# Kernel optimization log

Hardware: AMD Instinct MI355X
Metric: run time of the kernel (lower is better)

## Reference

```python
import jax, jax.numpy as jnp
import numpy as np

N = 100000      # nodes
E = 1600000     # edges (before self-loops)
IN = 128        # in_dim
HID = 128       # hidden_dim
H = 4           # heads
D = HID // H    # head_dim = 32
L = 3           # n_layers
G = 128         # graphs in batch
NEG_SLOPE = 0.2 # PyG GATConv default leaky_relu slope
BN_EPS = 1e-5


def setup_inputs() -> dict:
    key = jax.random.key(0)
    ks = jax.random.split(key, 16)
    x = jax.random.normal(ks[0], (N, IN), dtype=jnp.float32)
    edge_index = jax.random.randint(ks[1], (2, E), 0, N, dtype=jnp.int64)
    batch = jnp.sort(jax.random.randint(ks[2], (N,), 0, G, dtype=jnp.int64))
    # stacked per-layer GATConv params (in_dim == hidden_dim so all layers stack)
    W = jax.random.normal(ks[3], (L, HID, HID), dtype=jnp.float32) * (1.0 / np.sqrt(HID))
    att_src = jax.random.normal(ks[4], (L, H, D), dtype=jnp.float32) * 0.1
    att_dst = jax.random.normal(ks[5], (L, H, D), dtype=jnp.float32) * 0.1
    bias = jax.random.normal(ks[6], (L, HID), dtype=jnp.float32) * 0.01
    # BatchNorm1d (eval mode: running stats)
    gamma = 1.0 + 0.1 * jax.random.normal(ks[7], (L, HID), dtype=jnp.float32)
    beta = 0.01 * jax.random.normal(ks[8], (L, HID), dtype=jnp.float32)
    bn_mean = jnp.zeros((L, HID), dtype=jnp.float32)
    bn_var = jnp.ones((L, HID), dtype=jnp.float32)
    # MLP head: Linear(HID, HID//2) -> ReLU -> Linear(HID//2, 1)
    Wh1 = jax.random.normal(ks[9], (HID, HID // 2), dtype=jnp.float32) * (1.0 / np.sqrt(HID))
    bh1 = jnp.zeros((HID // 2,), dtype=jnp.float32)
    Wh2 = jax.random.normal(ks[10], (HID // 2, 1), dtype=jnp.float32) * (1.0 / np.sqrt(HID // 2))
    bh2 = jnp.zeros((1,), dtype=jnp.float32)
    return {"x": x, "edge_index": edge_index, "batch": batch, "W": W,
            "att_src": att_src, "att_dst": att_dst, "bias": bias,
            "gamma": gamma, "beta": beta, "bn_mean": bn_mean, "bn_var": bn_var,
            "Wh1": Wh1, "bh1": bh1, "Wh2": Wh2, "bh2": bh2}


def _gat_conv(x, src, dst, W_l, asrc, adst, b):
    # x: [N, F_in]; src/dst: [E+N] (self-loops included); returns [N, H*D]
    h = (x @ W_l).reshape(N, H, D)                      # [N,H,D]
    a_s = jnp.einsum('nhd,hd->nh', h, asrc)             # [N,H]
    a_d = jnp.einsum('nhd,hd->nh', h, adst)
    e = jax.nn.leaky_relu(a_s[src] + a_d[dst], NEG_SLOPE)  # [Etot,H]
    # segment softmax over incoming edges per destination node
    e_max = jax.ops.segment_max(e, dst, num_segments=N)    # [N,H]
    p = jnp.exp(e - e_max[dst])
    denom = jax.ops.segment_sum(p, dst, num_segments=N)    # [N,H]
    alpha = p / (denom[dst] + 1e-16)                        # [Etot,H]
    msg = h[src] * alpha[:, :, None]                        # [Etot,H,D]
    out = jax.ops.segment_sum(msg, dst, num_segments=N)     # [N,H,D]
    return out.reshape(N, H * D) + b


def reference(x, edge_index, batch, W, att_src, att_dst, bias,
              gamma, beta, bn_mean, bn_var, Wh1, bh1, Wh2, bh2):
    # add self-loops once (PyG GATConv default add_self_loops=True)
    loop = jnp.arange(N, dtype=edge_index.dtype)
    src = jnp.concatenate([edge_index[0], loop])
    dst = jnp.concatenate([edge_index[1], loop])
    for l in range(L):
        x = _gat_conv(x, src, dst, W[l], att_src[l], att_dst[l], bias[l])
        x = jnp.maximum(x, 0.0)
        # BatchNorm1d, eval mode (dropout is identity in eval)
        x = (x - bn_mean[l]) * (gamma[l] / jnp.sqrt(bn_var[l] + BN_EPS)) + beta[l]
    # global mean pool over graphs
    sums = jax.ops.segment_sum(x, batch, num_segments=G)            # [G,HID]
    cnts = jax.ops.segment_sum(jnp.ones((N,), x.dtype), batch, num_segments=G)
    pooled = sums / jnp.maximum(cnts, 1.0)[:, None]
    hdn = jnp.maximum(pooled @ Wh1 + bh1, 0.0)
    return (hdn @ Wh2 + bh2).squeeze(-1)                            # [G]
```

## Files before the change

kernel.cpp:

```cpp
#include <hip/hip_runtime.h>
#include <hip/hip_fp16.h>


typedef __bf16 bf16x8 __attribute__((ext_vector_type(8)));
typedef float  f32x4  __attribute__((ext_vector_type(4)));
typedef unsigned int u32x4 __attribute__((ext_vector_type(4)));

#define WLSZ 36864
#define MAXBKT 800
#define BCAP   4096

__global__ __launch_bounds__(256)
void k_bucket(const int* __restrict__ ei, unsigned int* __restrict__ bkt,
              int* __restrict__ bcnt, float* __restrict__ gsum,
              int* __restrict__ gcnt, int Ne, int Nn, int nbkt, int Gg) {
    __shared__ int lcnt[MAXBKT];
    __shared__ int lbase[MAXBKT];
    int tid = threadIdx.x;
    int gid = blockIdx.x * 256 + tid;
    if (gid < Gg * 128) gsum[gid] = 0.f;
    if (gid < Gg) gcnt[gid] = 0;
    for (int i = tid; i < nbkt; i += 256) lcnt[i] = 0;
    __syncthreads();
    int chunk0 = blockIdx.x * 2048;
    int nnz = Ne + Nn;
    for (int i = 0; i < 8; ++i) {
        int e = chunk0 + i * 256 + tid;
        if (e < nnz) {
            int d = (e < Ne) ? ei[Ne + e] : (e - Ne);
            atomicAdd(&lcnt[d >> 7], 1);
        }
    }
    __syncthreads();
    for (int b = tid; b < nbkt; b += 256) {
        int c = lcnt[b];
        lbase[b] = (c > 0) ? atomicAdd(&bcnt[b], c) : 0;
        lcnt[b] = 0;
    }
    __syncthreads();
    for (int i = 0; i < 8; ++i) {
        int e = chunk0 + i * 256 + tid;
        if (e < nnz) {
            int s, d;
            if (e < Ne) { s = ei[e]; d = ei[Ne + e]; }
            else        { s = e - Ne; d = e - Ne; }
            int b = d >> 7;
            int r = atomicAdd(&lcnt[b], 1);
            bkt[(long)b * BCAP + lbase[b] + r] = ((unsigned)s << 7) | (unsigned)(d & 127);
        }
    }
}

__global__ __launch_bounds__(1024)
void k_bktscan(const int* __restrict__ bcnt, int* __restrict__ bktbase, int nbkt) {
    __shared__ int s0[1024], s1[1024];
    int t = threadIdx.x;
    int v = (t < nbkt) ? bcnt[t] : 0;
    s0[t] = v;
    __syncthreads();
    int* src = s0; int* dst = s1;
    for (int off = 1; off < 1024; off <<= 1) {
        int x = src[t];
        if (t >= off) x += src[t - off];
        dst[t] = x;
        __syncthreads();
        int* tw = src; src = dst; dst = tw;
    }
    if (t < nbkt) bktbase[t] = src[t] - v;
}

__global__ __launch_bounds__(256)
void k_bscatter2(const unsigned int* __restrict__ bkt, const int* __restrict__ bcnt,
                 const int* __restrict__ bktbase, int* __restrict__ rowptr,
                 int* __restrict__ colv, int Nn, int nnz) {
    __shared__ int h[128], sc0[128], sc1[128];
    int b = blockIdx.x;
    int tid = threadIdx.x;
    if (tid < 128) h[tid] = 0;
    __syncthreads();
    int cnt = bcnt[b];
    int base = bktbase[b];
    const unsigned int* bp = bkt + (long)b * BCAP;
    for (int i = tid; i < cnt; i += 256) atomicAdd(&h[bp[i] & 127], 1);
    __syncthreads();
    if (tid < 128) sc0[tid] = h[tid];
    __syncthreads();
    int* src = sc0; int* dst = sc1;
    for (int off = 1; off < 128; off <<= 1) {
        if (tid < 128) {
            int x = src[tid];
            if (tid >= off) x += src[tid - off];
            dst[tid] = x;
        }
        __syncthreads();
        int* tw = src; src = dst; dst = tw;
    }
    int node = b * 128 + tid;
    if (tid < 128) {
        int excl = src[tid] - h[tid];
        int st = base + excl;
        h[tid] = st;
        if (node < Nn) rowptr[node] = st;
    }
    if (b == 0 && tid == 0) rowptr[Nn] = nnz;
    __syncthreads();
    for (int i = tid; i < cnt; i += 256) {
        unsigned int e = bp[i];
        int pos = atomicAdd(&h[e & 127], 1);
        colv[pos] = (int)(e >> 7);
    }
}

__device__ __forceinline__ int foff(int l, int d, int n, int k) {
    int ct = n >> 4, li = n & 15;
    int ks = k >> 5, bq = (k >> 3) & 3, j = k & 7;
    return l * WLSZ + (((ks * 18) + d * 9 + ct) * 64 + (bq << 4) + li) * 8 + j;
}

__global__ void k_prep(const float* __restrict__ gamma, const float* __restrict__ beta,
                       const float* __restrict__ mean, const float* __restrict__ var,
                       float* __restrict__ bn_mul, float* __restrict__ bn_add,
                       const float* __restrict__ W, const float* __restrict__ asrc,
                       const float* __restrict__ adst, __bf16* __restrict__ WF) {
    int gid = blockIdx.x * 256 + threadIdx.x;
    if (gid < 384) {
        float sc = gamma[gid] / sqrtf(var[gid] + 1e-5f);
        bn_mul[gid] = sc;
        bn_add[gid] = beta[gid] - mean[gid] * sc;
    }
    if (gid < 3 * 128 * 128) {
        int l = gid >> 14;
        int k = (gid >> 7) & 127;
        int n = gid & 127;
        float f = W[gid];
        __bf16 h = (__bf16)f;
        WF[foff(l, 0, n, k)] = h;
        WF[foff(l, 1, n, k)] = (__bf16)(f - (float)h);
    }
    if (gid < 3 * 128 * 8) {
        int l = gid >> 10;
        int r = gid & 1023;
        int k = r >> 3;
        int j = r & 7;
        int hh = j & 3;
        const float* av = (j < 4 ? asrc : adst) + l * 128 + hh * 32;
        const float* wp = W + l * 16384 + k * 128 + hh * 32;
        float sum = 0.f;
#pragma unroll
        for (int d = 0; d < 32; ++d) sum = fmaf(wp[d], av[d], sum);
        __bf16 h = (__bf16)sum;
        WF[foff(l, 0, 128 + j, k)] = h;
        WF[foff(l, 1, 128 + j, k)] = (__bf16)(sum - (float)h);
    }
    if (gid < 3 * 128 * 8) {
        int l = gid >> 10;
        int r = gid & 1023;
        int k = r >> 3;
        int j = r & 7;
        WF[foff(l, 0, 136 + j, k)] = (__bf16)0.f;
        WF[foff(l, 1, 136 + j, k)] = (__bf16)0.f;
    }
}

__global__ __launch_bounds__(256, 4)
void k_gemm_mfma(const float* __restrict__ X, const __bf16* __restrict__ WF,
                 __half* __restrict__ Hout,
                 float* __restrict__ as_, float* __restrict__ ad_, int Nn) {
    int t = threadIdx.x;
    int w = t >> 6;
    int lane = t & 63;
    int li = lane & 15;
    int b  = lane >> 4;
    long row = (long)blockIdx.x * 64 + w * 16 + li;
    long rA = (row > Nn - 1) ? (Nn - 1) : row;

    f32x4 acc[9];
#pragma unroll
    for (int ct = 0; ct < 9; ++ct) acc[ct] = (f32x4){0.f, 0.f, 0.f, 0.f};

#pragma unroll
    for (int ks = 0; ks < 4; ++ks) {
        int k0 = ks * 32 + 8 * b;
        const float* xp = X + rA * 128 + k0;
        float4 f0 = *(const float4*)xp;
        float4 f1 = *(const float4*)(xp + 4);
        float af[8] = {f0.x, f0.y, f0.z, f0.w, f1.x, f1.y, f1.z, f1.w};
        bf16x8 ahi, alo;
#pragma unroll
        for (int j = 0; j < 8; ++j) {
            __bf16 h = (__bf16)af[j];
            ahi[j] = h;
            alo[j] = (__bf16)(af[j] - (float)h);
        }
        const __bf16* wk = WF + (ks * 18) * 512 + lane * 8;
#pragma unroll
        for (int ct = 0; ct < 9; ++ct) {
            bf16x8 bhi = *(const bf16x8*)(wk + ct * 512);
            bf16x8 blo = *(const bf16x8*)(wk + (9 + ct) * 512);
            acc[ct] = __builtin_amdgcn_mfma_f32_16x16x32_bf16(bhi, ahi, acc[ct], 0, 0, 0);
            acc[ct] = __builtin_amdgcn_mfma_f32_16x16x32_bf16(bhi, alo, acc[ct], 0, 0, 0);
            acc[ct] = __builtin_amdgcn_mfma_f32_16x16x32_bf16(blo, ahi, acc[ct], 0, 0, 0);
        }
    }

    if (row < Nn) {
        __half* op = Hout + row * 128 + 4 * b;
#pragma unroll
        for (int ct = 0; ct < 8; ++ct) {
            union { __half2 h2[2]; uint2 u; } pk;
            pk.h2[0] = __floats2half2_rn(acc[ct][0], acc[ct][1]);
            pk.h2[1] = __floats2half2_rn(acc[ct][2], acc[ct][3]);
            *(uint2*)(op + ct * 16) = pk.u;
        }
        if (b == 0)
            *(float4*)(as_ + 4 * row) = make_float4(acc[8][0], acc[8][1],
                                                    acc[8][2], acc[8][3]);
        else if (b == 1)
            *(float4*)(ad_ + 4 * row) = make_float4(acc[8][0], acc[8][1],
                                                    acc[8][2], acc[8][3]);
    }
}

#define LEAKY(x) ((x) > 0.f ? (x) : 0.2f * (x))

__global__ __launch_bounds__(256)
void k_aggregate(const __half* __restrict__ Hb, const float* __restrict__ as_,
                 const float* __restrict__ ad_, const int* __restrict__ rowptr,
                 const int* __restrict__ col, const float* __restrict__ bias,
                 const float* __restrict__ bn_mul, const float* __restrict__ bn_add,
                 float* __restrict__ Xout, int Nn) {
    __shared__ int2 s_pk[4][64][4];
    int w = threadIdx.x >> 6;
    int n = (blockIdx.x << 2) + w;
    if (n >= Nn) return;
    int lane = threadIdx.x & 63;
    int start = rowptr[n], end = rowptr[n + 1];
    int deg = end - start;

    if (deg <= 64) {
        int hh = lane & 3;
        int slot = lane >> 2;
        float adn = ad_[4 * n + hh];
        float esc[4]; int scl[4];
#pragma unroll
        for (int c = 0; c < 4; ++c) {
            int eidx = (c << 4) + slot;
            float e = -1e30f; int s = 0;
            if (eidx < deg) {
                s = col[start + eidx];
                e = LEAKY(as_[4 * s + hh] + adn);
            }
            esc[c] = e; scl[c] = s;
        }
        float m = fmaxf(fmaxf(esc[0], esc[1]), fmaxf(esc[2], esc[3]));
#pragma unroll
        for (int msk = 4; msk < 64; msk <<= 1) m = fmaxf(m, __shfl_xor(m, msk, 64));
        float p[4];
        float den = 0.f;
#pragma unroll
        for (int c = 0; c < 4; ++c) { p[c] = __expf(esc[c] - m); den += p[c]; }
#pragma unroll
        for (int msk = 4; msk < 64; msk <<= 1) den += __shfl_xor(den, msk, 64);
        float inv = 1.f / (den + 1e-16f);
#pragma unroll
        for (int c = 0; c < 4; ++c) {
            int2 pk;
            pk.x = scl[c] << 8;
            pk.y = __float_as_int(p[c] * inv);
            s_pk[w][(c << 4) + slot][hh] = pk;
        }

        int quarter = lane >> 4;
        int li = lane & 15;
        int hB = li >> 2;
        int cByte = li << 4;
        const char* hb8 = (const char*)Hb;
        float acc[8];
#pragma unroll
        for (int i = 0; i < 8; ++i) acc[i] = 0.f;

        int nit = (deg + 7) >> 3;
        int2 pk0 = s_pk[w][quarter][hB];
        int2 pk1 = s_pk[w][quarter + 4][hB];
        float a0 = __int_as_float(pk0.y);
        float a1 = __int_as_float(pk1.y);
        u32x4 r0 = *(const u32x4*)(hb8 + pk0.x + cByte);
        u32x4 r1 = *(const u32x4*)(hb8 + pk1.x + cByte);
        for (int it = 1; it < nit; ++it) {
            int e0 = (it << 3) + quarter;
            int2 q0 = s_pk[w][e0][hB];
            int2 q1 = s_pk[w][e0 + 4][hB];
            u32x4 t0 = *(const u32x4*)(hb8 + q0.x + cByte);
            u32x4 t1 = *(const u32x4*)(hb8 + q1.x + cByte);
            const __half* h0 = (const __half*)&r0;
            const __half* h1 = (const __half*)&r1;
#pragma unroll
            for (int q = 0; q < 8; ++q) {
                acc[q] = fmaf(__half2float(h0[q]), a0, acc[q]);
                acc[q] = fmaf(__half2float(h1[q]), a1, acc[q]);
            }
            r0 = t0; r1 = t1;
            a0 = __int_as_float(q0.y);
            a1 = __int_as_float(q1.y);
        }
        {
            const __half* h0 = (const __half*)&r0;
            const __half* h1 = (const __half*)&r1;
#pragma unroll
            for (int q = 0; q < 8; ++q) {
                acc[q] = fmaf(__half2float(h0[q]), a0, acc[q]);
                acc[q] = fmaf(__half2float(h1[q]), a1, acc[q]);
            }
        }
#pragma unroll
        for (int i = 0; i < 8; ++i) {
            float v = acc[i];
            v += __shfl_xor(v, 16, 64);
            v += __shfl_xor(v, 32, 64);
            acc[i] = v;
        }
        if (lane < 16) {
            int c0 = li << 3;
            float4 bz0 = *(const float4*)(bias + c0);
            float4 bz1 = *(const float4*)(bias + c0 + 4);
            float4 m0 = *(const float4*)(bn_mul + c0);
            float4 m1 = *(const float4*)(bn_mul + c0 + 4);
            float4 a0v = *(const float4*)(bn_add + c0);
            float4 a1v = *(const float4*)(bn_add + c0 + 4);
            float4 o0, o1;
            o0.x = fmaf(fmaxf(acc[0] + bz0.x, 0.f), m0.x, a0v.x);
            o0.y = fmaf(fmaxf(acc[1] + bz0.y, 0.f), m0.y, a0v.y);
            o0.z = fmaf(fmaxf(acc[2] + bz0.z, 0.f), m0.z, a0v.z);
            o0.w = fmaf(fmaxf(acc[3] + bz0.w, 0.f), m0.w, a0v.w);
            o1.x = fmaf(fmaxf(acc[4] + bz1.x, 0.f), m1.x, a1v.x);
            o1.y = fmaf(fmaxf(acc[5] + bz1.y, 0.f), m1.y, a1v.y);
            o1.z = fmaf(fmaxf(acc[6] + bz1.z, 0.f), m1.z, a1v.z);
            o1.w = fmaf(fmaxf(acc[7] + bz1.w, 0.f), m1.w, a1v.w);
            *(float4*)(Xout + (long)n * 128 + c0)     = o0;
            *(float4*)(Xout + (long)n * 128 + c0 + 4) = o1;
        }
        return;
    }

    int hh = lane & 3;
    float adn = ad_[n * 4 + hh];
    float m = -1e30f;
    for (int base = start; base < end; base += 16) {
        int idx = base + (lane >> 2);
        float sc = -1e30f;
        if (idx < end) {
            int s = col[idx];
            float e = as_[s * 4 + hh] + adn;
            sc = LEAKY(e);
        }
        m = fmaxf(m, sc);
    }
    for (int msk = 4; msk < 64; msk <<= 1) m = fmaxf(m, __shfl_xor(m, msk, 64));
    float den = 0.f;
    for (int base = start; base < end; base += 16) {
        int idx = base + (lane >> 2);
        if (idx < end) {
            int s = col[idx];
            float e = as_[s * 4 + hh] + adn;
            e = LEAKY(e);
            den += __expf(e - m);
        }
    }
    for (int msk = 4; msk < 64; msk <<= 1) den += __shfl_xor(den, msk, 64);
    int hB = lane >> 4;
    float mB   = __shfl(m, hB, 64);
    float invB = 1.f / (__shfl(den, hB, 64) + 1e-16f);
    float adB  = ad_[n * 4 + hB];
    int c0 = lane << 1;
    float acc0 = 0.f, acc1 = 0.f;
    for (int i = start; i < end; ++i) {
        int s = col[i];
        float e = as_[s * 4 + hB] + adB;
        e = LEAKY(e);
        float alpha = __expf(e - mB) * invB;
        float2 hv = __half22float2(*(const __half2*)(Hb + (long)s * 128 + c0));
        acc0 = fmaf(hv.x, alpha, acc0);
        acc1 = fmaf(hv.y, alpha, acc1);
    }
    float v0 = acc0 + bias[c0], v1 = acc1 + bias[c0 + 1];
    v0 = fmaxf(v0, 0.f); v1 = fmaxf(v1, 0.f);
    v0 = fmaf(v0, bn_mul[c0], bn_add[c0]);
    v1 = fmaf(v1, bn_mul[c0 + 1], bn_add[c0 + 1]);
    *(float2*)(Xout + (long)n * 128 + c0) = make_float2(v0, v1);
}

__global__ __launch_bounds__(128)
void k_pool(const float* __restrict__ X, const int* __restrict__ batch,
            float* __restrict__ gsum, int* __restrict__ gcnt, int Nn) {
    int c = threadIdx.x;
    int n0 = blockIdx.x * 64;
    if (n0 >= Nn) return;
    int nend = (n0 + 64 < Nn) ? n0 + 64 : Nn;
    float local = 0.f;
    int gcur = batch[n0];
    int cnt = 0;
    for (int n = n0; n < nend; ++n) {
        int g = batch[n];
        if (g != gcur) {
            atomicAdd(&gsum[gcur * 128 + c], local);
            if (c == 0) atomicAdd(&gcnt[gcur], cnt);
            local = 0.f; cnt = 0; gcur = g;
        }
        local += X[(long)n * 128 + c];
        cnt += 1;
    }
    atomicAdd(&gsum[gcur * 128 + c], local);
    if (c == 0) atomicAdd(&gcnt[gcur], cnt);
}

__global__ __launch_bounds__(64)
void k_head(const float* __restrict__ gsum, const int* __restrict__ gcnt,
            const float* __restrict__ Wh1, const float* __restrict__ bh1,
            const float* __restrict__ Wh2, const float* __restrict__ bh2,
            float* __restrict__ outp) {
    __shared__ float pooled[128];
    int g = blockIdx.x;
    int j = threadIdx.x;
    int cnt = gcnt[g];
    float inv = 1.f / (float)(cnt > 1 ? cnt : 1);
    pooled[j]      = gsum[g * 128 + j] * inv;
    pooled[j + 64] = gsum[g * 128 + 64 + j] * inv;
    __syncthreads();
    float acc = bh1[j];
    for (int k = 0; k < 128; ++k) acc = fmaf(pooled[k], Wh1[k * 64 + j], acc);
    acc = fmaxf(acc, 0.f);
    float prod = acc * Wh2[j];
    for (int msk = 1; msk < 64; msk <<= 1) prod += __shfl_xor(prod, msk, 64);
    if (j == 0) outp[g] = prod + bh2[0];
}

extern "C" void kernel_launch(void* const* d_in, const int* in_sizes, int n_in,
                              void* d_out, int out_size, void* d_ws, size_t ws_size,
                              hipStream_t stream) {
    const float* x       = (const float*)d_in[0];
    const int*   ei      = (const int*)d_in[1];
    const int*   batch   = (const int*)d_in[2];
    const float* W       = (const float*)d_in[3];
    const float* att_src = (const float*)d_in[4];
    const float* att_dst = (const float*)d_in[5];
    const float* bias    = (const float*)d_in[6];
    const float* gamma   = (const float*)d_in[7];
    const float* beta    = (const float*)d_in[8];
    const float* bn_mean = (const float*)d_in[9];
    const float* bn_var  = (const float*)d_in[10];
    const float* Wh1     = (const float*)d_in[11];
    const float* bh1     = (const float*)d_in[12];
    const float* Wh2     = (const float*)d_in[13];
    const float* bh2     = (const float*)d_in[14];
    float* out = (float*)d_out;

    const int Nn = in_sizes[0] / 128;
    const int Ne = in_sizes[1] / 2;
    const int Gg = out_size;
    const int nnz = Ne + Nn;
    const int nbkt = (Nn + 127) / 128;

    char* ws = (char*)d_ws;
    size_t off = 0;
    auto alloc = [&](size_t bytes) -> char* {
        char* p = ws + off;
        off = (off + bytes + 255) & ~(size_t)255;
        return p;
    };
    float*        bufA    = (float*)alloc((size_t)Nn * 128 * 4);
    __half*       bufH    = (__half*)alloc((size_t)Nn * 128 * 2);
    float*        as_     = (float*)alloc((size_t)Nn * 4 * 4);
    float*        ad_     = (float*)alloc((size_t)Nn * 4 * 4);
    int*          rowptr  = (int*)alloc((size_t)(Nn + 1) * 4);
    int*          col     = (int*)alloc((size_t)nnz * 4);
    float*        bn_mul  = (float*)alloc(384 * 4);
    float*        bn_add  = (float*)alloc(384 * 4);
    float*        gsum    = (float*)alloc((size_t)Gg * 128 * 4);
    int*          gcnt    = (int*)alloc((size_t)Gg * 4);
    __bf16*       WtF     = (__bf16*)alloc((size_t)3 * WLSZ * 2);
    unsigned int* bkt     = (unsigned int*)alloc((size_t)nbkt * BCAP * 4);
    int*          bcnt    = (int*)alloc((size_t)nbkt * 4);
    int*          bktbase = (int*)alloc((size_t)nbkt * 4);

    hipMemsetAsync(bcnt, 0, (size_t)nbkt * 4, stream);
    k_prep<<<192, 256, 0, stream>>>(gamma, beta, bn_mean, bn_var, bn_mul, bn_add,
                                    W, att_src, att_dst, WtF);
    k_bucket<<<(nnz + 2047) / 2048, 256, 0, stream>>>(ei, bkt, bcnt, gsum, gcnt,
                                                      Ne, Nn, nbkt, Gg);
    k_bktscan<<<1, 1024, 0, stream>>>(bcnt, bktbase, nbkt);
    k_bscatter2<<<nbkt, 256, 0, stream>>>(bkt, bcnt, bktbase, rowptr, col, Nn, nnz);

    const float* cur = x;
    for (int l = 0; l < 3; ++l) {
        k_gemm_mfma<<<(Nn + 63) / 64, 256, 0, stream>>>(cur, WtF + l * WLSZ,
                                                        bufH, as_, ad_, Nn);
        k_aggregate<<<(Nn + 3) / 4, 256, 0, stream>>>(bufH, as_, ad_, rowptr, col,
                                                      bias + l * 128, bn_mul + l * 128,
                                                      bn_add + l * 128, bufA, Nn);
        cur = bufA;
    }

    k_pool<<<(Nn + 63) / 64, 128, 0, stream>>>(bufA, batch, gsum, gcnt, Nn);
    k_head<<<Gg, 64, 0, stream>>>(gsum, gcnt, Wh1, bh1, Wh2, bh2, out);
}
```

Baseline: 524.2 us.

## Fuse global mean pooling into last-layer aggregation and compute graph counts by binary search

The final aggregation kernel becomes a template with a pooling variant. For the last layer it no longer writes the 100000x128 activation matrix. Each block instead stages its four node outputs in shared memory and atomically adds them into per-graph sums, merging them into one add when all four nodes share a graph. Graph node counts come from a small binary-search kernel over the sorted batch array, which removes the separate pool kernel and its full re-read of the activations. The cost is an extra __syncthreads plus up to 128 global atomics per block, which will contend heavily on only 128 graphs.

```diff
diff --git a/kernel.cpp b/kernel.cpp
--- a/kernel.cpp
+++ b/kernel.cpp
@@ -111,6 +111,17 @@
     }
 }
 
+__global__ __launch_bounds__(128)
+void k_gcnt(const int* __restrict__ batch, int* __restrict__ gcnt, int Nn, int Gg) {
+    int g = threadIdx.x;
+    if (g >= Gg) return;
+    int lo = 0, hi = Nn;
+    while (lo < hi) { int mid = (lo + hi) >> 1; if (batch[mid] < g) lo = mid + 1; else hi = mid; }
+    int lo2 = lo, hi2 = Nn;
+    while (lo2 < hi2) { int mid = (lo2 + hi2) >> 1; if (batch[mid] < g + 1) lo2 = mid + 1; else hi2 = mid; }
+    gcnt[g] = lo2 - lo;
+}
+
 __device__ __forceinline__ int foff(int l, int d, int n, int k) {
     int ct = n >> 4, li = n & 15;
     int ks = k >> 5, bq = (k >> 3) & 3, j = k & 7;
@@ -223,194 +234,212 @@
 
 #define LEAKY(x) ((x) > 0.f ? (x) : 0.2f * (x))
 
+template <bool POOL>
 __global__ __launch_bounds__(256)
 void k_aggregate(const __half* __restrict__ Hb, const float* __restrict__ as_,
                  const float* __restrict__ ad_, const int* __restrict__ rowptr,
                  const int* __restrict__ col, const float* __restrict__ bias,
                  const float* __restrict__ bn_mul, const float* __restrict__ bn_add,
-                 float* __restrict__ Xout, int Nn) {
+                 float* __restrict__ Xout, const int* __restrict__ batch,
+                 float* __restrict__ gsum, int Nn) {
     __shared__ int2 s_pk[4][64][4];
+    __shared__ float s_out[POOL ? 4 : 1][POOL ? 128 : 1];
+    __shared__ int s_g[POOL ? 4 : 1];
     int w = threadIdx.x >> 6;
     int n = (blockIdx.x << 2) + w;
-    if (n >= Nn) return;
     int lane = threadIdx.x & 63;
-    int start = rowptr[n], end = rowptr[n + 1];
-    int deg = end - start;
-
-    if (deg <= 64) {
-        int hh = lane & 3;
-        int slot = lane >> 2;
-        float adn = ad_[4 * n + hh];
-        float esc[4]; int scl[4];
-#pragma unroll
-        for (int c = 0; c < 4; ++c) {
-            int eidx = (c << 4) + slot;
-            float e = -1e30f; int s = 0;
-            if (eidx < deg) {
-                s = col[start + eidx];
-                e = LEAKY(as_[4 * s + hh] + adn);
-            }
-            esc[c] = e; scl[c] = s;
-        }
-        float m = fmaxf(fmaxf(esc[0], esc[1]), fmaxf(esc[2], esc[3]));
-#pragma unroll
-        for (int msk = 4; msk < 64; msk <<= 1) m = fmaxf(m, __shfl_xor(m, msk, 64));
-        float p[4];
-        float den = 0.f;
-#pragma unroll
-        for (int c = 0; c < 4; ++c) { p[c] = __expf(esc[c] - m); den += p[c]; }
-#pragma unroll
-        for (int msk = 4; msk < 64; msk <<= 1) den += __shfl_xor(den, msk, 64);
-        float inv = 1.f / (den + 1e-16f);
-#pragma unroll
-        for (int c = 0; c < 4; ++c) {
-            int2 pk;
-            pk.x = scl[c] << 8;
-            pk.y = __float_as_int(p[c] * inv);
-            s_pk[w][(c << 4) + slot][hh] = pk;
-        }
-
-        int quarter = lane >> 4;
-        int li = lane & 15;
-        int hB = li >> 2;
-        int cByte = li << 4;
-        const char* hb8 = (const char*)Hb;
-        float acc[8];
-#pragma unroll
-        for (int i = 0; i < 8; ++i) acc[i] = 0.f;
-
-        int nit = (deg + 7) >> 3;
-        int2 pk0 = s_pk[w][quarter][hB];
-        int2 pk1 = s_pk[w][quarter + 4][hB];
-        float a0 = __int_as_float(pk0.y);
-        float a1 = __int_as_float(pk1.y);
-        u32x4 r0 = *(const u32x4*)(hb8 + pk0.x + cByte);
-        u32x4 r1 = *(const u32x4*)(hb8 + pk1.x + cByte);
-        for (int it = 1; it < nit; ++it) {
-            int e0 = (it << 3) + quarter;
-            int2 q0 = s_pk[w][e0][hB];
-            int2 q1 = s_pk[w][e0 + 4][hB];
-            u32x4 t0 = *(const u32x4*)(hb8 + q0.x + cByte);
-            u32x4 t1 = *(const u32x4*)(hb8 + q1.x + cByte);
-            const __half* h0 = (const __half*)&r0;
-            const __half* h1 = (const __half*)&r1;
-#pragma unroll
-            for (int q = 0; q < 8; ++q) {
-                acc[q] = fmaf(__half2float(h0[q]), a0, acc[q]);
-                acc[q] = fmaf(__half2float(h1[q]), a1, acc[q]);
-            }
-            r0 = t0; r1 = t1;
-            a0 = __int_as_float(q0.y);
-            a1 = __int_as_float(q1.y);
-        }
-        {
-            const __half* h0 = (const __half*)&r0;
-            const __half* h1 = (const __half*)&r1;
-#pragma unroll
-            for (int q = 0; q < 8; ++q) {
-                acc[q] = fmaf(__half2float(h0[q]), a0, acc[q]);
-                acc[q] = fmaf(__half2float(h1[q]), a1, acc[q]);
-            }
-        }
-#pragma unroll
-        for (int i = 0; i < 8; ++i) {
-            float v = acc[i];
-            v += __shfl_xor(v, 16, 64);
-            v += __shfl_xor(v, 32, 64);
-            acc[i] = v;
-        }
+    bool active = (n < Nn);
+    if (!POOL && !active) return;
+    if (POOL && lane == 0) s_g[w] = active ? batch[n] : -1;
+
+    if (active) {
+        int start = rowptr[n], end = rowptr[n + 1];
+        int deg = end - start;
+
+        if (deg <= 64) {
+            int hh = lane & 3;
+            int slot = lane >> 2;
+            float adn = ad_[4 * n + hh];
+            float esc[4]; int scl[4];
+#pragma unroll
+            for (int c = 0; c < 4; ++c) {
+                int eidx = (c << 4) + slot;
+                float e = -1e30f; int s = 0;
+                if (eidx < deg) {
+                    s = col[start + eidx];
+                    e = LEAKY(as_[4 * s + hh] + adn);
+                }
+                esc[c] = e; scl[c] = s;
+            }
+            float m = fmaxf(fmaxf(esc[0], esc[1]), fmaxf(esc[2], esc[3]));
+#pragma unroll
+            for (int msk = 4; msk < 64; msk <<= 1) m = fmaxf(m, __shfl_xor(m, msk, 64));
+            float p[4];
+            float den = 0.f;
+#pragma unroll
+            for (int c = 0; c < 4; ++c) { p[c] = __expf(esc[c] - m); den += p[c]; }
+#pragma unroll
+            for (int msk = 4; msk < 64; msk <<= 1) den += __shfl_xor(den, msk, 64);
+            float inv = 1.f / (den + 1e-16f);
+#pragma unroll
+            for (int c = 0; c < 4; ++c) {
+                int2 pk;
+                pk.x = scl[c] << 8;
+                pk.y = __float_as_int(p[c] * inv);
+                s_pk[w][(c << 4) + slot][hh] = pk;
+            }
+
+            int quarter = lane >> 4;
+            int li = lane & 15;
+            int hB = li >> 2;
+            int cByte = li << 4;
+            const char* hb8 = (const char*)Hb;
+            float acc[8];
+#pragma unroll
+            for (int i = 0; i < 8; ++i) acc[i] = 0.f;
+
+            int nit = (deg + 7) >> 3;
+            int2 pk0 = s_pk[w][quarter][hB];
+            int2 pk1 = s_pk[w][quarter + 4][hB];
+            float a0 = __int_as_float(pk0.y);
+            float a1 = __int_as_float(pk1.y);
+            u32x4 r0 = *(const u32x4*)(hb8 + pk0.x + cByte);
+            u32x4 r1 = *(const u32x4*)(hb8 + pk1.x + cByte);
+            for (int it = 1; it < nit; ++it) {
+                int e0 = (it << 3) + quarter;
+                int2 q0 = s_pk[w][e0][hB];
+                int2 q1 = s_pk[w][e0 + 4][hB];
+                u32x4 t0 = *(const u32x4*)(hb8 + q0.x + cByte);
+                u32x4 t1 = *(const u32x4*)(hb8 + q1.x + cByte);
+                const __half* h0 = (const __half*)&r0;
+                const __half* h1 = (const __half*)&r1;
+#pragma unroll
+                for (int q = 0; q < 8; ++q) {
+                    acc[q] = fmaf(__half2float(h0[q]), a0, acc[q]);
+                    acc[q] = fmaf(__half2float(h1[q]), a1, acc[q]);
+                }
+                r0 = t0; r1 = t1;
+                a0 = __int_as_float(q0.y);
+                a1 = __int_as_float(q1.y);
+            }
+            {
+                const __half* h0 = (const __half*)&r0;
+                const __half* h1 = (const __half*)&r1;
+#pragma unroll
+                for (int q = 0; q < 8; ++q) {
+                    acc[q] = fmaf(__half2float(h0[q]), a0, acc[q]);
+                    acc[q] = fmaf(__half2float(h1[q]), a1, acc[q]);
+                }
+            }
+#pragma unroll
+            for (int i = 0; i < 8; ++i) {
+                float v = acc[i];
+                v += __shfl_xor(v, 16, 64);
+                v += __shfl_xor(v, 32, 64);
+                acc[i] = v;
+            }
+            if (lane < 16) {
+                int c0 = li << 3;
+                float4 bz0 = *(const float4*)(bias + c0);
+                float4 bz1 = *(const float4*)(bias + c0 + 4);
+                float4 m0 = *(const float4*)(bn_mul + c0);
+                float4 m1 = *(const float4*)(bn_mul + c0 + 4);
+                float4 a0v = *(const float4*)(bn_add + c0);
+                float4 a1v = *(const float4*)(bn_add + c0 + 4);
+                float4 o0, o1;
+                o0.x = fmaf(fmaxf(acc[0] + bz0.x, 0.f), m0.x, a0v.x);
+                o0.y = fmaf(fmaxf(acc[1] + bz0.y, 0.f), m0.y, a0v.y);
+                o0.z = fmaf(fmaxf(acc[2] + bz0.z, 0.f), m0.z, a0v.z);
+                o0.w = fmaf(fmaxf(acc[3] + bz0.w, 0.f), m0.w, a0v.w);
+                o1.x = fmaf(fmaxf(acc[4] + bz1.x, 0.f), m1.x, a1v.x);
+                o1.y = fmaf(fmaxf(acc[5] + bz1.y, 0.f), m1.y, a1v.y);
+                o1.z = fmaf(fmaxf(acc[6] + bz1.z, 0.f), m1.z, a1v.z);
+                o1.w = fmaf(fmaxf(acc[7] + bz1.w, 0.f), m1.w, a1v.w);
+                if (!POOL) {
+                    *(float4*)(Xout + (long)n * 128 + c0)     = o0;
+                    *(float4*)(Xout + (long)n * 128 + c0 + 4) = o1;
+                } else {
+                    *(float4*)(&s_out[w][c0])     = o0;
+                    *(float4*)(&s_out[w][c0 + 4]) = o1;
+                }
+            }
+        } else {
+            int hh = lane & 3;
+            float adn = ad_[n * 4 + hh];
+            float m = -1e30f;
+            for (int base = start; base < end; base += 16) {
+                int idx = base + (lane >> 2);
+                float sc = -1e30f;
+                if (idx < end) {
+                    int s = col[idx];
+                    float e = as_[s * 4 + hh] + adn;
+                    sc = LEAKY(e);
+                }
+                m = fmaxf(m, sc);
+            }
+            for (int msk = 4; msk < 64; msk <<= 1) m = fmaxf(m, __shfl_xor(m, msk, 64));
+            float den = 0.f;
+            for (int base = start; base < end; base += 16) {
+                int idx = base + (lane >> 2);
+                if (idx < end) {
+                    int s = col[idx];
+                    float e = as_[s * 4 + hh] + adn;
+                    e = LEAKY(e);
+                    den += __expf(e - m);
+                }
+            }
+            for (int msk = 4; msk < 64; msk <<= 1) den += __shfl_xor(den, msk, 64);
+            int hB = lane >> 4;
+            float mB   = __shfl(m, hB, 64);
+            float invB = 1.f / (__shfl(den, hB, 64) + 1e-16f);
+            float adB  = ad_[n * 4 + hB];
+            int c0 = lane << 1;
+            float acc0 = 0.f, acc1 = 0.f;
+            for (int i = start; i < end; ++i) {
+                int s = col[i];
+                float e = as_[s * 4 + hB] + adB;
+                e = LEAKY(e);
+                float alpha = __expf(e - mB) * invB;
+                float2 hv = __half22float2(*(const __half2*)(Hb + (long)s * 128 + c0));
+                acc0 = fmaf(hv.x, alpha, acc0);
+                acc1 = fmaf(hv.y, alpha, acc1);
+            }
+            float v0 = acc0 + bias[c0], v1 = acc1 + bias[c0 + 1];
+            v0 = fmaxf(v0, 0.f); v1 = fmaxf(v1, 0.f);
+            v0 = fmaf(v0, bn_mul[c0], bn_add[c0]);
+            v1 = fmaf(v1, bn_mul[c0 + 1], bn_add[c0 + 1]);
+            if (!POOL) {
+                *(float2*)(Xout + (long)n * 128 + c0) = make_float2(v0, v1);
+            } else {
+                s_out[w][c0]     = v0;
+                s_out[w][c0 + 1] = v1;
+            }
+        }
+    } else if (POOL) {
         if (lane < 16) {
-            int c0 = li << 3;
-            float4 bz0 = *(const float4*)(bias + c0);
-            float4 bz1 = *(const float4*)(bias + c0 + 4);
-            float4 m0 = *(const float4*)(bn_mul + c0);
-            float4 m1 = *(const float4*)(bn_mul + c0 + 4);
-            float4 a0v = *(const float4*)(bn_add + c0);
-            float4 a1v = *(const float4*)(bn_add + c0 + 4);
-            float4 o0, o1;
-            o0.x = fmaf(fmaxf(acc[0] + bz0.x, 0.f), m0.x, a0v.x);
-            o0.y = fmaf(fmaxf(acc[1] + bz0.y, 0.f), m0.y, a0v.y);
-            o0.z = fmaf(fmaxf(acc[2] + bz0.z, 0.f), m0.z, a0v.z);
-            o0.w = fmaf(fmaxf(acc[3] + bz0.w, 0.f), m0.w, a0v.w);
-            o1.x = fmaf(fmaxf(acc[4] + bz1.x, 0.f), m1.x, a1v.x);
-            o1.y = fmaf(fmaxf(acc[5] + bz1.y, 0.f), m1.y, a1v.y);
-            o1.z = fmaf(fmaxf(acc[6] + bz1.z, 0.f), m1.z, a1v.z);
-            o1.w = fmaf(fmaxf(acc[7] + bz1.w, 0.f), m1.w, a1v.w);
-            *(float4*)(Xout + (long)n * 128 + c0)     = o0;
-            *(float4*)(Xout + (long)n * 128 + c0 + 4) = o1;
-        }
-        return;
-    }
-
-    int hh = lane & 3;
-    float adn = ad_[n * 4 + hh];
-    float m = -1e30f;
-    for (int base = start; base < end; base += 16) {
-        int idx = base + (lane >> 2);
-        float sc = -1e30f;
-        if (idx < end) {
-            int s = col[idx];
-            float e = as_[s * 4 + hh] + adn;
-            sc = LEAKY(e);
-        }
-        m = fmaxf(m, sc);
-    }
-    for (int msk = 4; msk < 64; msk <<= 1) m = fmaxf(m, __shfl_xor(m, msk, 64));
-    float den = 0.f;
-    for (int base = start; base < end; base += 16) {
-        int idx = base + (lane >> 2);
-        if (idx < end) {
-            int s = col[idx];
-            float e = as_[s * 4 + hh] + adn;
-            e = LEAKY(e);
-            den += __expf(e - m);
-        }
-    }
-    for (int msk = 4; msk < 64; msk <<= 1) den += __shfl_xor(den, msk, 64);
-    int hB = lane >> 4;
-    float mB   = __shfl(m, hB, 64);
-    float invB = 1.f / (__shfl(den, hB, 64) + 1e-16f);
-    float adB  = ad_[n * 4 + hB];
-    int c0 = lane << 1;
-    float acc0 = 0.f, acc1 = 0.f;
-    for (int i = start; i < end; ++i) {
-        int s = col[i];
-        float e = as_[s * 4 + hB] + adB;
-        e = LEAKY(e);
-        float alpha = __expf(e - mB) * invB;
-        float2 hv = __half22float2(*(const __half2*)(Hb + (long)s * 128 + c0));
-        acc0 = fmaf(hv.x, alpha, acc0);
-        acc1 = fmaf(hv.y, alpha, acc1);
-    }
-    float v0 = acc0 + bias[c0], v1 = acc1 + bias[c0 + 1];
-    v0 = fmaxf(v0, 0.f); v1 = fmaxf(v1, 0.f);
-    v0 = fmaf(v0, bn_mul[c0], bn_add[c0]);
-    v1 = fmaf(v1, bn_mul[c0 + 1], bn_add[c0 + 1]);
-    *(float2*)(Xout + (long)n * 128 + c0) = make_float2(v0, v1);
-}
-
-__global__ __launch_bounds__(128)
-void k_pool(const float* __restrict__ X, const int* __restrict__ batch,
-            float* __restrict__ gsum, int* __restrict__ gcnt, int Nn) {
-    int c = threadIdx.x;
-    int n0 = blockIdx.x * 64;
-    if (n0 >= Nn) return;
-    int nend = (n0 + 64 < Nn) ? n0 + 64 : Nn;
-    float local = 0.f;
-    int gcur = batch[n0];
-    int cnt = 0;
-    for (int n = n0; n < nend; ++n) {
-        int g = batch[n];
-        if (g != gcur) {
-            atomicAdd(&gsum[gcur * 128 + c], local);
-            if (c == 0) atomicAdd(&gcnt[gcur], cnt);
-            local = 0.f; cnt = 0; gcur = g;
-        }
-        local += X[(long)n * 128 + c];
-        cnt += 1;
-    }
-    atomicAdd(&gsum[gcur * 128 + c], local);
-    if (c == 0) atomicAdd(&gcnt[gcur], cnt);
+            int c0 = (lane & 15) << 3;
+#pragma unroll
+            for (int i = 0; i < 8; ++i) s_out[w][c0 + i] = 0.f;
+        }
+    }
+
+    if (POOL) {
+        __syncthreads();
+        int tid = threadIdx.x;
+        if (tid < 128) {
+            int g0 = s_g[0], g1 = s_g[1], g2 = s_g[2], g3 = s_g[3];
+            float v0 = s_out[0][tid], v1 = s_out[1][tid];
+            float v2 = s_out[2][tid], v3 = s_out[3][tid];
+            if (g0 == g1 && g1 == g2 && g2 == g3) {
+                if (g0 >= 0) atomicAdd(&gsum[g0 * 128 + tid], v0 + v1 + v2 + v3);
+            } else {
+                if (g0 >= 0) atomicAdd(&gsum[g0 * 128 + tid], v0);
+                if (g1 >= 0) atomicAdd(&gsum[g1 * 128 + tid], v1);
+                if (g2 >= 0) atomicAdd(&gsum[g2 * 128 + tid], v2);
+                if (g3 >= 0) atomicAdd(&gsum[g3 * 128 + tid], v3);
+            }
+        }
+    }
 }
 
 __global__ __launch_bounds__(64)
@@ -487,6 +516,7 @@
                                     W, att_src, att_dst, WtF);
     k_bucket<<<(nnz + 2047) / 2048, 256, 0, stream>>>(ei, bkt, bcnt, gsum, gcnt,
                                                       Ne, Nn, nbkt, Gg);
+    k_gcnt<<<1, 128, 0, stream>>>(batch, gcnt, Nn, Gg);
     k_bktscan<<<1, 1024, 0, stream>>>(bcnt, bktbase, nbkt);
     k_bscatter2<<<nbkt, 256, 0, stream>>>(bkt, bcnt, bktbase, rowptr, col, Nn, nnz);
 
@@ -494,12 +524,16 @@
     for (int l = 0; l < 3; ++l) {
         k_gemm_mfma<<<(Nn + 63) / 64, 256, 0, stream>>>(cur, WtF + l * WLSZ,
                                                         bufH, as_, ad_, Nn);
-        k_aggregate<<<(Nn + 3) / 4, 256, 0, stream>>>(bufH, as_, ad_, rowptr, col,
-                                                      bias + l * 128, bn_mul + l * 128,
-                                                      bn_add + l * 128, bufA, Nn);
+        if (l < 2)
+            k_aggregate<false><<<(Nn + 3) / 4, 256, 0, stream>>>(
+                bufH, as_, ad_, rowptr, col, bias + l * 128, bn_mul + l * 128,
+                bn_add + l * 128, bufA, batch, gsum, Nn);
+        else
+            k_aggregate<true><<<(Nn + 3) / 4, 256, 0, stream>>>(
+                bufH, as_, ad_, rowptr, col, bias + l * 128, bn_mul + l * 128,
+                bn_add + l * 128, bufA, batch, gsum, Nn);
         cur = bufA;
     }
 
-    k_pool<<<(Nn + 63) / 64, 128, 0, stream>>>(bufA, batch, gsum, gcnt, Nn);
     k_head<<<Gg, 64, 0, stream>>>(gsum, gcnt, Wh1, bh1, Wh2, bh2, out);
 }
```

Result: no change. 525.3 us (+0.2%).
